# Optimization experiments

Hardware: AMD Instinct MI355X
Metric: run time of the kernel (lower is better)

## Reference

```python
import jax, jax.numpy as jnp
import numpy as np

N_NODES = 100000
NEG_SLOPE = 0.01  # F.leaky_relu default


def setup_inputs() -> dict:
    key = jax.random.key(0)
    k1, k2, k3, k4, k5 = jax.random.split(key, 5)
    x = jax.random.normal(k1, (N_NODES, 128), dtype=jnp.float32)
    edge_index = jax.random.randint(k2, (2, 1600000), 0, N_NODES, dtype=jnp.int64)
    # GCNConv linear weights (PyG: x @ W.T), bias added after aggregation
    W1 = jax.random.normal(k3, (128, 128), dtype=jnp.float32) * (1.0 / np.sqrt(128))
    b1 = jnp.zeros((128,), dtype=jnp.float32)
    W2 = jax.random.normal(k4, (128, 128), dtype=jnp.float32) * (1.0 / np.sqrt(128))
    b2 = jnp.zeros((128,), dtype=jnp.float32)
    return {"x": x, "edge_index": edge_index, "W1": W1, "b1": b1, "W2": W2, "b2": b2}


def _gcn_layer(x, W, b, src, dst, norm, self_w):
    # linear transform first (GCNConv order): h = x @ W.T
    h = x @ W.T
    # message passing: sum_j norm_ij * h_j  (edges) + self-loop term h_i / deg_i
    msg = h[src] * norm[:, None]                       # [E, F] gather (memory-bound)
    agg = jax.ops.segment_sum(msg, dst, num_segments=x.shape[0])
    out = agg + h * self_w[:, None] + b
    return out


def reference(x, edge_index, W1, b1, W2, b2):
    src = edge_index[0]
    dst = edge_index[1]
    n = x.shape[0]
    # gcn_norm with self-loops: deg_i = in-degree(dst) + 1
    deg = jax.ops.segment_sum(jnp.ones_like(dst, dtype=x.dtype), dst, num_segments=n) + 1.0
    deg_inv_sqrt = jax.lax.rsqrt(deg)
    norm = deg_inv_sqrt[src] * deg_inv_sqrt[dst]       # edge weights
    self_w = deg_inv_sqrt * deg_inv_sqrt               # self-loop weight = 1/deg

    h = _gcn_layer(x, W1, b1, src, dst, norm, self_w)
    h = jax.nn.leaky_relu(h, NEG_SLOPE)
    # dropout inactive (eval semantics)
    h = _gcn_layer(h, W2, b2, src, dst, norm, self_w)
    h = jax.nn.leaky_relu(h, NEG_SLOPE)
    return h
```

## Files before the change

### kernel.cpp

```cpp
#include <hip/hip_runtime.h>

#define F 128
#define NEG_SLOPE 0.01f
#define NPB 512
#define PMAX 256
#define HB 8192
#define BB 8192
#define CAP 12288

typedef _Float16 half8_t __attribute__((ext_vector_type(8)));
typedef _Float16 half4_t __attribute__((ext_vector_type(4)));
typedef float f32x4 __attribute__((ext_vector_type(4)));


__global__ __launch_bounds__(512) void zero_bcnt(int* __restrict__ bcnt,
                                                 int* __restrict__ bcur) {
    int tid = threadIdx.x;
    if (tid < PMAX) bcnt[tid] = 0;
    else bcur[tid - PMAX] = 0;
}

__global__ __launch_bounds__(256) void hist_kernel(const int* __restrict__ dst,
                                                   int* __restrict__ bcnt,
                                                   int E, int nP,
                                                   const float* __restrict__ W1,
                                                   const float* __restrict__ W2,
                                                   _Float16* __restrict__ W1h,
                                                   _Float16* __restrict__ W2h) {
    __shared__ int h[PMAX];
    int tid = threadIdx.x;
    int hb = gridDim.x - 32;
    if (blockIdx.x >= hb) {
        int i = (blockIdx.x - hb) * 256 + tid;
        const int n4 = F * F / 4;
        const float* in = (i < n4) ? W1 : W2;
        _Float16* out = (i < n4) ? W1h : W2h;
        int j = (i < n4) ? i : i - n4;
        float4 v = ((const float4*)in)[j];
        half8_t hx;
        hx[0] = (_Float16)v.x; hx[1] = (_Float16)v.y;
        hx[2] = (_Float16)v.z; hx[3] = (_Float16)v.w;
        *(int2*)&((_Float16*)out)[j * 4] = *(int2*)&hx;
        return;
    }
    if (tid < PMAX) h[tid] = 0;
    __syncthreads();
    int base = blockIdx.x * HB;
    for (int i = tid; i < HB && base + i < E; i += 256)
        atomicAdd(&h[dst[base + i] >> 9], 1);
    __syncthreads();
    if (tid < nP && h[tid]) atomicAdd(&bcnt[tid], h[tid]);
}

__global__ __launch_bounds__(256) void bin_kernel(const int* __restrict__ src,
                                                  const int* __restrict__ dst,
                                                  const int* __restrict__ bcnt,
                                                  int* __restrict__ bcur,
                                                  int* __restrict__ bbase,
                                                  int* __restrict__ binned,
                                                  int E, int nP) {
    __shared__ int hist[PMAX];
    __shared__ int lbase[PMAX];
    __shared__ int gbase[PMAX];
    __shared__ int cur[PMAX];
    __shared__ int sa[PMAX];
    __shared__ int sb[PMAX];
    __shared__ int buf[BB];
    __shared__ unsigned char b8[BB];
    int tid = threadIdx.x;
    int base = blockIdx.x * BB;
    int myE = E - base; if (myE > BB) myE = BB;

    hist[tid] = 0;
    __syncthreads();
    for (int i = tid; i < myE; i += 256)
        atomicAdd(&hist[dst[base + i] >> 9], 1);
    __syncthreads();
    {
        int v = (tid < nP) ? hist[tid] : 0;
        int run = v;
        sa[tid] = v;
        __syncthreads();
        for (int off = 1; off < PMAX; off <<= 1) {
            int add = (tid >= off) ? sa[tid - off] : 0;
            __syncthreads();
            run += add;
            sa[tid] = run;
            __syncthreads();
        }
        if (tid < nP) { lbase[tid] = run - v; cur[tid] = run - v; }
    }
    {
        int v = (tid < nP) ? bcnt[tid] : 0;
        int run = v;
        sb[tid] = v;
        __syncthreads();
        for (int off = 1; off < PMAX; off <<= 1) {
            int add = (tid >= off) ? sb[tid - off] : 0;
            __syncthreads();
            run += add;
            sb[tid] = run;
            __syncthreads();
        }
        int gexc = run - v;
        if (tid < nP) {
            if (blockIdx.x == 0) bbase[tid] = gexc;
            gbase[tid] = hist[tid] ? gexc + atomicAdd(&bcur[tid], hist[tid]) : 0;
        }
    }
    __syncthreads();
    for (int i = tid; i < myE; i += 256) {
        int d = dst[base + i], s = src[base + i];
        int b = d >> 9;
        int lp = atomicAdd(&cur[b], 1);
        buf[lp] = ((d & (NPB - 1)) << 17) | s;
        b8[lp] = (unsigned char)b;
    }
    __syncthreads();
    for (int j = tid; j < myE; j += 256) {
        int b = b8[j];
        binned[gbase[b] + (j - lbase[b])] = buf[j];
    }
}

__global__ __launch_bounds__(256) void csr_kernel(const int* __restrict__ binned,
                                                  const int* __restrict__ bcnt,
                                                  const int* __restrict__ bbase,
                                                  int* __restrict__ srcs,
                                                  int* __restrict__ offs,
                                                  float* __restrict__ dis, int N) {
    __shared__ int cnt[NPB];
    __shared__ int tmp[NPB];
    __shared__ int cur[NPB];
    __shared__ int buf[CAP];
    int tid = threadIdx.x;
    int b = blockIdx.x;
    int ebase = bbase[b];
    int count = bcnt[b];
    int lo = b << 9;
    cnt[tid] = 0;
    cnt[tid + 256] = 0;
    __syncthreads();
    for (int j = tid; j < count; j += 256)
        atomicAdd(&cnt[binned[ebase + j] >> 17], 1);
    __syncthreads();
    int j0 = tid, j1 = tid + 256;
    int v0 = cnt[j0], v1 = cnt[j1];
    tmp[j0] = v0; tmp[j1] = v1;
    __syncthreads();
    for (int off = 1; off < NPB; off <<= 1) {
        int t0 = tmp[j0] + (j0 >= off ? tmp[j0 - off] : 0);
        int t1 = tmp[j1] + (j1 >= off ? tmp[j1 - off] : 0);
        __syncthreads();
        tmp[j0] = t0; tmp[j1] = t1;
        __syncthreads();
    }
    int e0 = tmp[j0] - v0, e1 = tmp[j1] - v1;
    cur[j0] = e0; cur[j1] = e1;
    int n0 = lo + j0, n1 = lo + j1;
    if (n0 < N) { offs[n0] = ebase + e0; dis[n0] = rsqrtf((float)v0 + 1.0f); }
    if (n1 < N) { offs[n1] = ebase + e1; dis[n1] = rsqrtf((float)v1 + 1.0f); }
    __syncthreads();
    for (int j = tid; j < count; j += 256) {
        int rec = binned[ebase + j];
        int pos = atomicAdd(&cur[rec >> 17], 1);
        int s = rec & 0x1FFFF;
        if (pos < CAP) buf[pos] = s; else srcs[ebase + pos] = s;
    }
    __syncthreads();
    int lim = count < CAP ? count : CAP;
    for (int j = tid; j < lim; j += 256)
        srcs[ebase + j] = buf[j];
}


__global__ __launch_bounds__(256) void gemm_a32(const float* __restrict__ A,
                                                const _Float16* __restrict__ Wh,
                                                const float* __restrict__ dis,
                                                _Float16* __restrict__ out,
                                                int ntiles) {
    int wave = threadIdx.x >> 6;
    int lane = threadIdx.x & 63;
    int tile = blockIdx.x * 4 + wave;
    if (tile >= ntiles) return;
    int m = lane & 15, quad = lane >> 4;
    const float* arow = A + (size_t)tile * 16 * F;
    half8_t afrag[4];
#pragma unroll
    for (int c = 0; c < 4; ++c) {
        f32x4 t0 = __builtin_nontemporal_load(
            (const f32x4*)&arow[m * F + c * 32 + quad * 8]);
        f32x4 t1 = __builtin_nontemporal_load(
            (const f32x4*)&arow[m * F + c * 32 + quad * 8 + 4]);
        afrag[c][0] = (_Float16)t0[0]; afrag[c][1] = (_Float16)t0[1];
        afrag[c][2] = (_Float16)t0[2]; afrag[c][3] = (_Float16)t0[3];
        afrag[c][4] = (_Float16)t1[0]; afrag[c][5] = (_Float16)t1[1];
        afrag[c][6] = (_Float16)t1[2]; afrag[c][7] = (_Float16)t1[3];
    }
    f32x4 acc[8];
#pragma unroll
    for (int t = 0; t < 8; ++t) acc[t] = (f32x4){0.f, 0.f, 0.f, 0.f};
#pragma unroll
    for (int c = 0; c < 4; ++c) {
#pragma unroll
        for (int t = 0; t < 8; ++t) {
            half8_t bfrag = *(const half8_t*)&Wh[(t * 16 + m) * F + c * 32 + quad * 8];
            acc[t] = __builtin_amdgcn_mfma_f32_16x16x32_f16(afrag[c], bfrag, acc[t],
                                                            0, 0, 0);
        }
    }
    float d[4];
#pragma unroll
    for (int r = 0; r < 4; ++r) d[r] = dis[tile * 16 + quad * 4 + r];
    _Float16* orow = out + (size_t)tile * 16 * F;
#pragma unroll
    for (int t = 0; t < 8; ++t)
#pragma unroll
        for (int r = 0; r < 4; ++r)
            orow[(quad * 4 + r) * F + t * 16 + m] = (_Float16)(acc[t][r] * d[r]);
}


__global__ __launch_bounds__(256) void agg_gemm16(const half8_t* __restrict__ h8,
                                                  const float* __restrict__ dis,
                                                  const float* __restrict__ bias,
                                                  const _Float16* __restrict__ Wh,
                                                  const int* __restrict__ srcs,
                                                  const int* __restrict__ offs,
                                                  _Float16* __restrict__ out,
                                                  int n, int E) {
    __shared__ _Float16 Af[16 * F];
    int tile = blockIdx.x;
    int w = threadIdx.x >> 6;
    int lane = threadIdx.x & 63;
    int g = lane >> 4;
    int fo = lane & 15;
    float4 b0 = ((const float4*)bias)[fo * 2];
    float4 b1v = ((const float4*)bias)[fo * 2 + 1];

#pragma unroll
    for (int i = 0; i < 4; ++i) {
        int row = w * 4 + i;
        int node = tile * 16 + row;
        float acc[8];
#pragma unroll
        for (int j = 0; j < 8; ++j) acc[j] = 0.f;
        int beg = 0, end = 0;
        float di = 0.f;
        half8_t hv = {};
        if (node < n) {
            beg = offs[node];
            end = (node + 1 < n) ? offs[node + 1] : E;
            di = dis[node];
            hv = h8[(size_t)node * 16 + fo];
        }
        if (beg < end) {
            int i0 = beg + g, i1 = beg + 4 + g;
            int s0 = srcs[i0 < end ? i0 : beg];
            int s1 = srcs[i1 < end ? i1 : beg];
            float w0 = (i0 < end) ? 1.f : 0.f;
            float w1 = (i1 < end) ? 1.f : 0.f;
            for (int e = beg; e < end; e += 8) {
                int ns0 = s0, ns1 = s1;
                float nw0 = 0.f, nw1 = 0.f;
                if (e + 8 < end) {
                    int j0 = e + 8 + g, j1 = e + 12 + g;
                    ns0 = srcs[j0 < end ? j0 : beg];
                    ns1 = srcs[j1 < end ? j1 : beg];
                    nw0 = (j0 < end) ? 1.f : 0.f;
                    nw1 = (j1 < end) ? 1.f : 0.f;
                }
                half8_t a0 = h8[(size_t)s0 * 16 + fo];
                half8_t a1 = h8[(size_t)s1 * 16 + fo];
#pragma unroll
                for (int j = 0; j < 8; ++j)
                    acc[j] += w0 * (float)a0[j] + w1 * (float)a1[j];
                s0 = ns0; s1 = ns1; w0 = nw0; w1 = nw1;
            }
        }
#pragma unroll
        for (int j = 0; j < 8; ++j) {
            acc[j] += __shfl_xor(acc[j], 16);
            acc[j] += __shfl_xor(acc[j], 32);
        }
        if (lane < 16) {
            half8_t o = {};
            if (node < n) {
                acc[0] = di * (acc[0] + (float)hv[0]) + b0.x;
                acc[1] = di * (acc[1] + (float)hv[1]) + b0.y;
                acc[2] = di * (acc[2] + (float)hv[2]) + b0.z;
                acc[3] = di * (acc[3] + (float)hv[3]) + b0.w;
                acc[4] = di * (acc[4] + (float)hv[4]) + b1v.x;
                acc[5] = di * (acc[5] + (float)hv[5]) + b1v.y;
                acc[6] = di * (acc[6] + (float)hv[6]) + b1v.z;
                acc[7] = di * (acc[7] + (float)hv[7]) + b1v.w;
#pragma unroll
                for (int j = 0; j < 8; ++j) {
                    float v = (acc[j] > 0.f) ? acc[j] : acc[j] * NEG_SLOPE;
                    o[j] = (_Float16)v;
                }
            }
            int cs = fo ^ (row & 7);
            *(half8_t*)&Af[row * F + cs * 8] = o;
        }
    }
    __syncthreads();

    int m = fo, quad = g;
    half8_t bfragA[4];
#pragma unroll
    for (int c = 0; c < 4; ++c)
        bfragA[c] = *(const half8_t*)&Af[fo * F + ((c * 4 + quad) ^ (fo & 7)) * 8];
    int onode = tile * 16 + fo;
    float di2 = (onode < n) ? dis[onode] : 0.f;
#pragma unroll
    for (int s = 0; s < 2; ++s) {
        int t = w * 2 + s;
        f32x4 acc2 = (f32x4){0.f, 0.f, 0.f, 0.f};
#pragma unroll
        for (int c = 0; c < 4; ++c) {
            half8_t afragW = *(const half8_t*)&Wh[(t * 16 + m) * F + c * 32 + quad * 8];
            acc2 = __builtin_amdgcn_mfma_f32_16x16x32_f16(afragW, bfragA[c], acc2,
                                                          0, 0, 0);
        }
        half4_t o4;
#pragma unroll
        for (int r = 0; r < 4; ++r) o4[r] = (_Float16)(acc2[r] * di2);
        if (onode < n)
            *(half4_t*)&out[(size_t)onode * F + t * 16 + quad * 4] = o4;
    }
}


__global__ __launch_bounds__(256) void agg_to_f(const half8_t* __restrict__ h8,
                                                const float* __restrict__ dis,
                                                const float* __restrict__ bias,
                                                const int* __restrict__ srcs,
                                                const int* __restrict__ offs,
                                                float* __restrict__ out,
                                                int n, int E) {
    int node = blockIdx.x * 4 + (threadIdx.x >> 6);
    int lane = threadIdx.x & 63;
    if (node >= n) return;
    int g = lane >> 4;
    int fo = lane & 15;
    int beg = offs[node];
    int end = (node + 1 < n) ? offs[node + 1] : E;
    float di = dis[node];
    half8_t hv = h8[(size_t)node * 16 + fo];
    float4 b0 = ((const float4*)bias)[fo * 2];
    float4 b1v = ((const float4*)bias)[fo * 2 + 1];
    float acc[8];
#pragma unroll
    for (int j = 0; j < 8; ++j) acc[j] = 0.f;
    if (beg < end) {
        int i0 = beg + g, i1 = beg + 4 + g;
        int s0 = __builtin_nontemporal_load(&srcs[i0 < end ? i0 : beg]);
        int s1 = __builtin_nontemporal_load(&srcs[i1 < end ? i1 : beg]);
        float w0 = (i0 < end) ? 1.f : 0.f;
        float w1 = (i1 < end) ? 1.f : 0.f;
        for (int e = beg; e < end; e += 8) {
            int ns0 = s0, ns1 = s1;
            float nw0 = 0.f, nw1 = 0.f;
            if (e + 8 < end) {
                int j0 = e + 8 + g, j1 = e + 12 + g;
                ns0 = __builtin_nontemporal_load(&srcs[j0 < end ? j0 : beg]);
                ns1 = __builtin_nontemporal_load(&srcs[j1 < end ? j1 : beg]);
                nw0 = (j0 < end) ? 1.f : 0.f;
                nw1 = (j1 < end) ? 1.f : 0.f;
            }
            half8_t a0 = h8[(size_t)s0 * 16 + fo];
            half8_t a1 = h8[(size_t)s1 * 16 + fo];
#pragma unroll
            for (int j = 0; j < 8; ++j)
                acc[j] += w0 * (float)a0[j] + w1 * (float)a1[j];
            s0 = ns0; s1 = ns1; w0 = nw0; w1 = nw1;
        }
    }
#pragma unroll
    for (int j = 0; j < 8; ++j) {
        acc[j] += __shfl_xor(acc[j], 16);
        acc[j] += __shfl_xor(acc[j], 32);
    }
    if (lane >= 16) return;
    acc[0] = di * (acc[0] + (float)hv[0]) + b0.x;
    acc[1] = di * (acc[1] + (float)hv[1]) + b0.y;
    acc[2] = di * (acc[2] + (float)hv[2]) + b0.z;
    acc[3] = di * (acc[3] + (float)hv[3]) + b0.w;
    acc[4] = di * (acc[4] + (float)hv[4]) + b1v.x;
    acc[5] = di * (acc[5] + (float)hv[5]) + b1v.y;
    acc[6] = di * (acc[6] + (float)hv[6]) + b1v.z;
    acc[7] = di * (acc[7] + (float)hv[7]) + b1v.w;
#pragma unroll
    for (int j = 0; j < 8; ++j)
        acc[j] = (acc[j] > 0.f) ? acc[j] : acc[j] * NEG_SLOPE;
    f32x4 o0 = (f32x4){acc[0], acc[1], acc[2], acc[3]};
    f32x4 o1 = (f32x4){acc[4], acc[5], acc[6], acc[7]};
    __builtin_nontemporal_store(o0, (f32x4*)out + (size_t)node * 32 + fo * 2);
    __builtin_nontemporal_store(o1, (f32x4*)out + (size_t)node * 32 + fo * 2 + 1);
}


static inline size_t alup(size_t x) { return (x + 255) & ~(size_t)255; }

extern "C" void kernel_launch(void* const* d_in, const int* in_sizes, int n_in,
                              void* d_out, int out_size, void* d_ws, size_t ws_size,
                              hipStream_t stream) {
    const float* x  = (const float*)d_in[0];
    const int*   ei = (const int*)d_in[1];
    const float* W1 = (const float*)d_in[2];
    const float* b1 = (const float*)d_in[3];
    const float* W2 = (const float*)d_in[4];
    const float* b2 = (const float*)d_in[5];
    float* out = (float*)d_out;

    const int N = in_sizes[0] / F;
    const int E = in_sizes[1] / 2;
    const int* src = ei;
    const int* dst = ei + E;

    char* p = (char*)d_ws;
    int*      bcnt   = (int*)p;      p += alup(PMAX * 4);
    int*      bbase  = (int*)p;      p += alup(PMAX * 4);
    int*      bcur   = (int*)p;      p += alup(PMAX * 4);
    float*    dis    = (float*)p;    p += alup((size_t)N * 4);
    int*      offs   = (int*)p;      p += alup((size_t)N * 4);
    int*      binned = (int*)p;      p += alup((size_t)E * 4);
    int*      srcs   = (int*)p;      p += alup((size_t)E * 4);
    _Float16* g      = (_Float16*)p; p += alup((size_t)N * F * 2);
    _Float16* hh     = (_Float16*)p; p += alup((size_t)N * F * 2);
    _Float16* W1h    = (_Float16*)p; p += alup((size_t)F * F * 2);
    _Float16* W2h    = (_Float16*)p; p += alup((size_t)F * F * 2);

    const int nP = (N + NPB - 1) / NPB;
    const int ntiles = (N + 15) / 16;
    const int gemm_grid = (ntiles + 3) / 4;
    const int agg_grid = (N + 3) / 4;

    zero_bcnt<<<1, 512, 0, stream>>>(bcnt, bcur);
    hist_kernel<<<(E + HB - 1) / HB + 32, 256, 0, stream>>>(dst, bcnt, E, nP,
                                                            W1, W2, W1h, W2h);
    bin_kernel<<<(E + BB - 1) / BB, 256, 0, stream>>>(src, dst, bcnt, bcur,
                                                      bbase, binned, E, nP);
    csr_kernel<<<nP, 256, 0, stream>>>(binned, bcnt, bbase, srcs, offs, dis, N);

    gemm_a32<<<gemm_grid, 256, 0, stream>>>(x, W1h, dis, hh, ntiles);
    agg_gemm16<<<ntiles, 256, 0, stream>>>((const half8_t*)hh, dis, b1, W2h,
                                           srcs, offs, g, N, E);
    agg_to_f<<<agg_grid, 256, 0, stream>>>((const half8_t*)g, dis, b2, srcs,
                                           offs, out, N, E);
}
```

Before: 329.7 us.

## Use zero-padded sentinel row and fma_mix accumulation in gather-aggregate loops

Adds a zeroed extra row at index N in both fp16 feature buffers and points out-of-range edge slots at it, which removes the per-edge 0/1 weight multiplies. Inner accumulation now uses inline-asm v_fma_mix_f32 to add fp16 halves straight into fp32 accumulators without separate conversions. Nontemporal loads and stores in the GEMM and final aggregation kernels are replaced with ordinary cached accesses. The padded rows add a little workspace and a small zeroing step inside the histogram kernel.

Result: no change. 327.4 us (-0.7%).

```diff
diff --git a/kernel.cpp b/kernel.cpp
--- a/kernel.cpp
+++ b/kernel.cpp
@@ -12,6 +12,15 @@
 typedef _Float16 half4_t __attribute__((ext_vector_type(4)));
 typedef float f32x4 __attribute__((ext_vector_type(4)));
 
+#define MIX_ACC(j, reg, sel)                                                   \
+    asm("v_fma_mix_f32 %0, %1, %2, %0 op_sel:[" sel ",0,0] op_sel_hi:[1,0,0]"  \
+        : "+v"(acc[j]) : "v"(reg), "v"(one));
+#define MIX_ROW(a)                                                             \
+    MIX_ACC(0, a.x, "0") MIX_ACC(1, a.x, "1")                                  \
+    MIX_ACC(2, a.y, "0") MIX_ACC(3, a.y, "1")                                  \
+    MIX_ACC(4, a.z, "0") MIX_ACC(5, a.z, "1")                                  \
+    MIX_ACC(6, a.w, "0") MIX_ACC(7, a.w, "1")
+
 
 __global__ __launch_bounds__(512) void zero_bcnt(int* __restrict__ bcnt,
                                                  int* __restrict__ bcur) {
@@ -26,11 +35,17 @@
                                                    const float* __restrict__ W1,
                                                    const float* __restrict__ W2,
                                                    _Float16* __restrict__ W1h,
-                                                   _Float16* __restrict__ W2h) {
+                                                   _Float16* __restrict__ W2h,
+                                                   _Float16* __restrict__ hpad,
+                                                   _Float16* __restrict__ gpad) {
     __shared__ int h[PMAX];
     int tid = threadIdx.x;
     int hb = gridDim.x - 32;
     if (blockIdx.x >= hb) {
+        if (blockIdx.x == hb) {
+            if (tid < 64) ((int*)hpad)[tid] = 0;
+            else if (tid < 128) ((int*)gpad)[tid - 64] = 0;
+        }
         int i = (blockIdx.x - hb) * 256 + tid;
         const int n4 = F * F / 4;
         const float* in = (i < n4) ? W1 : W2;
@@ -188,14 +203,12 @@
     half8_t afrag[4];
 #pragma unroll
     for (int c = 0; c < 4; ++c) {
-        f32x4 t0 = __builtin_nontemporal_load(
-            (const f32x4*)&arow[m * F + c * 32 + quad * 8]);
-        f32x4 t1 = __builtin_nontemporal_load(
-            (const f32x4*)&arow[m * F + c * 32 + quad * 8 + 4]);
-        afrag[c][0] = (_Float16)t0[0]; afrag[c][1] = (_Float16)t0[1];
-        afrag[c][2] = (_Float16)t0[2]; afrag[c][3] = (_Float16)t0[3];
-        afrag[c][4] = (_Float16)t1[0]; afrag[c][5] = (_Float16)t1[1];
-        afrag[c][6] = (_Float16)t1[2]; afrag[c][7] = (_Float16)t1[3];
+        float4 t0 = *(const float4*)&arow[m * F + c * 32 + quad * 8];
+        float4 t1 = *(const float4*)&arow[m * F + c * 32 + quad * 8 + 4];
+        afrag[c][0] = (_Float16)t0.x; afrag[c][1] = (_Float16)t0.y;
+        afrag[c][2] = (_Float16)t0.z; afrag[c][3] = (_Float16)t0.w;
+        afrag[c][4] = (_Float16)t1.x; afrag[c][5] = (_Float16)t1.y;
+        afrag[c][6] = (_Float16)t1.z; afrag[c][7] = (_Float16)t1.w;
     }
     f32x4 acc[8];
 #pragma unroll
@@ -235,6 +248,7 @@
     int lane = threadIdx.x & 63;
     int g = lane >> 4;
     int fo = lane & 15;
+    float one = 1.0f;
     float4 b0 = ((const float4*)bias)[fo * 2];
     float4 b1v = ((const float4*)bias)[fo * 2 + 1];
 
@@ -256,26 +270,20 @@
         }
         if (beg < end) {
             int i0 = beg + g, i1 = beg + 4 + g;
-            int s0 = srcs[i0 < end ? i0 : beg];
-            int s1 = srcs[i1 < end ? i1 : beg];
-            float w0 = (i0 < end) ? 1.f : 0.f;
-            float w1 = (i1 < end) ? 1.f : 0.f;
+            int s0 = (i0 < end) ? srcs[i0] : n;
+            int s1 = (i1 < end) ? srcs[i1] : n;
             for (int e = beg; e < end; e += 8) {
-                int ns0 = s0, ns1 = s1;
-                float nw0 = 0.f, nw1 = 0.f;
+                int ns0 = n, ns1 = n;
                 if (e + 8 < end) {
                     int j0 = e + 8 + g, j1 = e + 12 + g;
-                    ns0 = srcs[j0 < end ? j0 : beg];
-                    ns1 = srcs[j1 < end ? j1 : beg];
-                    nw0 = (j0 < end) ? 1.f : 0.f;
-                    nw1 = (j1 < end) ? 1.f : 0.f;
+                    ns0 = (j0 < end) ? srcs[j0] : n;
+                    ns1 = (j1 < end) ? srcs[j1] : n;
                 }
-                half8_t a0 = h8[(size_t)s0 * 16 + fo];
-                half8_t a1 = h8[(size_t)s1 * 16 + fo];
-#pragma unroll
-                for (int j = 0; j < 8; ++j)
-                    acc[j] += w0 * (float)a0[j] + w1 * (float)a1[j];
-                s0 = ns0; s1 = ns1; w0 = nw0; w1 = nw1;
+                int4 a0 = *(const int4*)&h8[(size_t)s0 * 16 + fo];
+                int4 a1 = *(const int4*)&h8[(size_t)s1 * 16 + fo];
+                MIX_ROW(a0)
+                MIX_ROW(a1)
+                s0 = ns0; s1 = ns1;
             }
         }
 #pragma unroll
@@ -347,6 +355,7 @@
     int beg = offs[node];
     int end = (node + 1 < n) ? offs[node + 1] : E;
     float di = dis[node];
+    float one = 1.0f;
     half8_t hv = h8[(size_t)node * 16 + fo];
     float4 b0 = ((const float4*)bias)[fo * 2];
     float4 b1v = ((const float4*)bias)[fo * 2 + 1];
@@ -355,26 +364,20 @@
     for (int j = 0; j < 8; ++j) acc[j] = 0.f;
     if (beg < end) {
         int i0 = beg + g, i1 = beg + 4 + g;
-        int s0 = __builtin_nontemporal_load(&srcs[i0 < end ? i0 : beg]);
-        int s1 = __builtin_nontemporal_load(&srcs[i1 < end ? i1 : beg]);
-        float w0 = (i0 < end) ? 1.f : 0.f;
-        float w1 = (i1 < end) ? 1.f : 0.f;
+        int s0 = (i0 < end) ? srcs[i0] : n;
+        int s1 = (i1 < end) ? srcs[i1] : n;
         for (int e = beg; e < end; e += 8) {
-            int ns0 = s0, ns1 = s1;
-            float nw0 = 0.f, nw1 = 0.f;
+            int ns0 = n, ns1 = n;
             if (e + 8 < end) {
                 int j0 = e + 8 + g, j1 = e + 12 + g;
-                ns0 = __builtin_nontemporal_load(&srcs[j0 < end ? j0 : beg]);
-                ns1 = __builtin_nontemporal_load(&srcs[j1 < end ? j1 : beg]);
-                nw0 = (j0 < end) ? 1.f : 0.f;
-                nw1 = (j1 < end) ? 1.f : 0.f;
+                ns0 = (j0 < end) ? srcs[j0] : n;
+                ns1 = (j1 < end) ? srcs[j1] : n;
             }
-            half8_t a0 = h8[(size_t)s0 * 16 + fo];
-            half8_t a1 = h8[(size_t)s1 * 16 + fo];
-#pragma unroll
-            for (int j = 0; j < 8; ++j)
-                acc[j] += w0 * (float)a0[j] + w1 * (float)a1[j];
-            s0 = ns0; s1 = ns1; w0 = nw0; w1 = nw1;
+            int4 a0 = *(const int4*)&h8[(size_t)s0 * 16 + fo];
+            int4 a1 = *(const int4*)&h8[(size_t)s1 * 16 + fo];
+            MIX_ROW(a0)
+            MIX_ROW(a1)
+            s0 = ns0; s1 = ns1;
         }
     }
 #pragma unroll
@@ -394,10 +397,10 @@
 #pragma unroll
     for (int j = 0; j < 8; ++j)
         acc[j] = (acc[j] > 0.f) ? acc[j] : acc[j] * NEG_SLOPE;
-    f32x4 o0 = (f32x4){acc[0], acc[1], acc[2], acc[3]};
-    f32x4 o1 = (f32x4){acc[4], acc[5], acc[6], acc[7]};
-    __builtin_nontemporal_store(o0, (f32x4*)out + (size_t)node * 32 + fo * 2);
-    __builtin_nontemporal_store(o1, (f32x4*)out + (size_t)node * 32 + fo * 2 + 1);
+    float4 o0 = make_float4(acc[0], acc[1], acc[2], acc[3]);
+    float4 o1 = make_float4(acc[4], acc[5], acc[6], acc[7]);
+    ((float4*)out)[(size_t)node * 32 + fo * 2] = o0;
+    ((float4*)out)[(size_t)node * 32 + fo * 2 + 1] = o1;
 }
 
 
@@ -427,8 +430,8 @@
     int*      offs   = (int*)p;      p += alup((size_t)N * 4);
     int*      binned = (int*)p;      p += alup((size_t)E * 4);
     int*      srcs   = (int*)p;      p += alup((size_t)E * 4);
-    _Float16* g      = (_Float16*)p; p += alup((size_t)N * F * 2);
-    _Float16* hh     = (_Float16*)p; p += alup((size_t)N * F * 2);
+    _Float16* g      = (_Float16*)p; p += alup(((size_t)N + 1) * F * 2);
+    _Float16* hh     = (_Float16*)p; p += alup(((size_t)N + 1) * F * 2);
     _Float16* W1h    = (_Float16*)p; p += alup((size_t)F * F * 2);
     _Float16* W2h    = (_Float16*)p; p += alup((size_t)F * F * 2);
 
@@ -438,8 +441,9 @@
     const int agg_grid = (N + 3) / 4;
 
     zero_bcnt<<<1, 512, 0, stream>>>(bcnt, bcur);
-    hist_kernel<<<(E + HB - 1) / HB + 32, 256, 0, stream>>>(dst, bcnt, E, nP,
-                                                            W1, W2, W1h, W2h);
+    hist_kernel<<<(E + HB - 1) / HB + 32, 256, 0, stream>>>(
+        dst, bcnt, E, nP, W1, W2, W1h, W2h,
+        hh + (size_t)N * F, g + (size_t)N * F);
     bin_kernel<<<(E + BB - 1) / BB, 256, 0, stream>>>(src, dst, bcnt, bcur,
                                                       bbase, binned, E, nP);
     csr_kernel<<<nP, 256, 0, stream>>>(binned, bcnt, bbase, srcs, offs, dis, N);
```
